# Optimization experiments

Hardware: AMD Instinct MI355X
Metric: run time of the kernel (lower is better)

## Reference

```python
import jax, jax.numpy as jnp
import numpy as np

LN_EPS = 1e-5


def _layernorm(x, w, b):
    mu = jnp.mean(x, axis=-1, keepdims=True)
    var = jnp.mean(jnp.square(x - mu), axis=-1, keepdims=True)
    return (x - mu) * jax.lax.rsqrt(var + LN_EPS) * w + b


def setup_inputs() -> dict:
    key = jax.random.key(0)
    ks = jax.random.split(key, 6)
    B, V, P, D = 32, 4, 784, 768
    H = 8
    x = jax.random.normal(ks[0], (B, V * P, D), dtype=jnp.float32)
    s = 0.02  # init scale for weights
    return {
        "x": x,
        "num_views": V,
        "norm1_w": jnp.ones((D,), jnp.float32),
        "norm1_b": jnp.zeros((D,), jnp.float32),
        "in_proj_w": jax.random.normal(ks[1], (3 * D, D), jnp.float32) * s,
        "in_proj_b": jnp.zeros((3 * D,), jnp.float32),
        "out_w": jax.random.normal(ks[2], (D, D), jnp.float32) * s,
        "out_b": jnp.zeros((D,), jnp.float32),
        "norm2_w": jnp.ones((D,), jnp.float32),
        "norm2_b": jnp.zeros((D,), jnp.float32),
        "ffn_w1": jax.random.normal(ks[3], (4 * D, D), jnp.float32) * s,
        "ffn_b1": jnp.zeros((4 * D,), jnp.float32),
        "ffn_w2": jax.random.normal(ks[4], (D, 4 * D), jnp.float32) * s,
        "ffn_b2": jnp.zeros((D,), jnp.float32),
    }


def reference(x, num_views, norm1_w, norm1_b, in_proj_w, in_proj_b, out_w, out_b,
              norm2_w, norm2_b, ffn_w1, ffn_b1, ffn_w2, ffn_b2):
    B, T, D = x.shape
    V = num_views
    P = T // V
    H = 8
    dh = D // H

    # The per-patch python loop in the original is embarrassingly parallel over
    # patches: fold the patch dim into batch -> (B*P, V, D) tokens of seq-len V.
    xv = x.reshape(B, V, P, D).transpose(0, 2, 1, 3).reshape(B * P, V, D)

    # pre-norm cross-view attention (torch MultiheadAttention, batch_first)
    h = _layernorm(xv, norm1_w, norm1_b)
    qkv = h @ in_proj_w.T + in_proj_b                      # (BP, V, 3D)
    q, k, v = jnp.split(qkv, 3, axis=-1)
    q = q.reshape(B * P, V, H, dh).transpose(0, 2, 1, 3)   # (BP, H, V, dh)
    k = k.reshape(B * P, V, H, dh).transpose(0, 2, 1, 3)
    v = v.reshape(B * P, V, H, dh).transpose(0, 2, 1, 3)
    scores = jnp.einsum("bhqd,bhkd->bhqk", q, k) / jnp.sqrt(jnp.float32(dh))
    attn = jax.nn.softmax(scores, axis=-1)
    o = jnp.einsum("bhqk,bhkd->bhqd", attn, v)             # (BP, H, V, dh)
    o = o.transpose(0, 2, 1, 3).reshape(B * P, V, D)
    o = o @ out_w.T + out_b
    xv = xv + o

    # pre-norm FFN with exact (erf) GELU; dropout = identity (eval mode)
    h = _layernorm(xv, norm2_w, norm2_b)
    h = jax.nn.gelu(h @ ffn_w1.T + ffn_b1, approximate=False)
    xv = xv + (h @ ffn_w2.T + ffn_b2)

    # undo the fold: (BP, V, D) -> (B, P, V, D) -> (B, V, P, D) -> (B, T, D)
    return xv.reshape(B, P, V, D).transpose(0, 2, 1, 3).reshape(B, T, D)
```

## Files before the change

kernel.cpp:

```cpp
#include <hip/hip_runtime.h>
#include <hip/hip_bf16.h>
#include <math.h>

typedef __bf16 bf16x8 __attribute__((ext_vector_type(8)));
typedef float  f32x4  __attribute__((ext_vector_type(4)));
typedef unsigned short us8 __attribute__((ext_vector_type(8)));
typedef unsigned short us4 __attribute__((ext_vector_type(4)));

__device__ __forceinline__ unsigned short f2bf(float x) {
  unsigned int u = __float_as_uint(x);
  u += 0x7FFFu + ((u >> 16) & 1u);
  return (unsigned short)(u >> 16);
}
__device__ __forceinline__ float bf2f(unsigned short v) {
  return __uint_as_float(((unsigned int)v) << 16);
}
__device__ __forceinline__ float gelu_t(float x) {
  float y = 0.7978845608028654f * x * (1.0f + 0.044715f * x * x);
  float e = __expf(2.0f * y);
  return x - x / (e + 1.0f);
}


__global__ __launch_bounds__(256) void conv_f32_bf16(const float* __restrict__ s,
                                                     unsigned short* __restrict__ d, int n4) {
  int i = blockIdx.x * 256 + threadIdx.x;
  if (i >= n4) return;
  float4 f = ((const float4*)s)[i];
  ushort4 u;
  u.x = f2bf(f.x); u.y = f2bf(f.y); u.z = f2bf(f.z); u.w = f2bf(f.w);
  ((ushort4*)d)[i] = u;
}

__global__ __launch_bounds__(256) void ln_kernel(const float* __restrict__ src,
                                                 const float* __restrict__ w,
                                                 const float* __restrict__ b,
                                                 unsigned short* __restrict__ dst) {
  const int wv = threadIdx.x >> 6;
  const int lane = threadIdx.x & 63;
  const int n = blockIdx.x * 4 + wv;
  const int bp = n >> 2, v = n & 3;
  const int bb = bp / 784, p = bp - bb * 784;
  const float* row = src + ((size_t)bb * 3136 + (size_t)v * 784 + p) * 768;
  float4 x0 = ((const float4*)row)[lane];
  float4 x1 = ((const float4*)row)[lane + 64];
  float4 x2 = ((const float4*)row)[lane + 128];
  float s  = x0.x + x0.y + x0.z + x0.w + x1.x + x1.y + x1.z + x1.w
           + x2.x + x2.y + x2.z + x2.w;
  float ss = x0.x*x0.x + x0.y*x0.y + x0.z*x0.z + x0.w*x0.w
           + x1.x*x1.x + x1.y*x1.y + x1.z*x1.z + x1.w*x1.w
           + x2.x*x2.x + x2.y*x2.y + x2.z*x2.z + x2.w*x2.w;
  #pragma unroll
  for (int off = 32; off > 0; off >>= 1) {
    s  += __shfl_xor(s,  off, 64);
    ss += __shfl_xor(ss, off, 64);
  }
  const float mu   = s * (1.0f / 768.0f);
  const float rstd = rsqrtf(ss * (1.0f / 768.0f) - mu * mu + 1e-5f);
  unsigned short* drow = dst + (size_t)n * 768;
  #pragma unroll
  for (int seg = 0; seg < 3; ++seg) {
    float4 xs = (seg == 0) ? x0 : (seg == 1) ? x1 : x2;
    float4 w4 = ((const float4*)w)[lane + seg * 64];
    float4 b4 = ((const float4*)b)[lane + seg * 64];
    ushort4 u;
    u.x = f2bf((xs.x - mu) * rstd * w4.x + b4.x);
    u.y = f2bf((xs.y - mu) * rstd * w4.y + b4.y);
    u.z = f2bf((xs.z - mu) * rstd * w4.z + b4.z);
    u.w = f2bf((xs.w - mu) * rstd * w4.w + b4.w);
    ((ushort4*)drow)[lane + seg * 64] = u;
  }
}

template <int K, int EPI>
__global__ __launch_bounds__(256) void gemm_k(const unsigned short* __restrict__ A,
                                              const unsigned short* __restrict__ Bm,
                                              const float* __restrict__ bias,
                                              void* __restrict__ outp,
                                              const float* __restrict__ aux,
                                              int N) {
  __shared__ unsigned short smem[2 * 128 * 64];
  unsigned short* sA = smem;
  unsigned short* sB = smem + 128 * 64;
  const int tid  = threadIdx.x;
  const int w    = tid >> 6;
  const int lane = tid & 63;
  const int quad = lane >> 4;
  const int l16  = lane & 15;
  const int wm = w >> 1, wn = w & 1;

  const int gx   = gridDim.x;
  const int flat = blockIdx.y * gx + blockIdx.x;
  const int xcd  = flat & 7;
  const int idx  = flat >> 3;
  const int iby  = idx / gx;
  const int by   = xcd * 98 + iby;
  const int bx   = idx - iby * gx;

  const int r8 = lane >> 3;
  const int cb = lane & 7;
  const int swo = ((cb ^ r8) << 3);
  const unsigned short* gA = A  + (size_t)(by * 128 + r8) * K + swo;
  const unsigned short* gB = Bm + (size_t)(bx * 128 + r8) * K + swo;

  f32x4 acc[4][4];
  #pragma unroll
  for (int i = 0; i < 4; ++i)
    #pragma unroll
    for (int j = 0; j < 4; ++j) {
      f32x4 z = {0.0f, 0.0f, 0.0f, 0.0f};
      acc[i][j] = z;
    }

  for (int k0 = 0; k0 < K; k0 += 64) {
    #pragma unroll
    for (int i = 0; i < 4; ++i) {
      const int chunk = w * 4 + i;
      __builtin_amdgcn_global_load_lds(
          (__attribute__((address_space(1))) void*)(gA + (size_t)(chunk * 8) * K + k0),
          (__attribute__((address_space(3))) void*)(&sA[chunk * 512]), 16, 0, 0);
      __builtin_amdgcn_global_load_lds(
          (__attribute__((address_space(1))) void*)(gB + (size_t)(chunk * 8) * K + k0),
          (__attribute__((address_space(3))) void*)(&sB[chunk * 512]), 16, 0, 0);
    }
    __syncthreads();

    #pragma unroll
    for (int kk = 0; kk < 2; ++kk) {
      bf16x8 af[4], bfr[4];
      const int q = kk * 4 + quad;
      #pragma unroll
      for (int mi = 0; mi < 4; ++mi) {
        const int m = wm * 64 + mi * 16 + l16;
        af[mi] = *(const bf16x8*)(&sA[m * 64 + ((q ^ (m & 7)) << 3)]);
      }
      #pragma unroll
      for (int ni = 0; ni < 4; ++ni) {
        const int n = wn * 64 + ni * 16 + l16;
        bfr[ni] = *(const bf16x8*)(&sB[n * 64 + ((q ^ (n & 7)) << 3)]);
      }
      #pragma unroll
      for (int mi = 0; mi < 4; ++mi)
        #pragma unroll
        for (int ni = 0; ni < 4; ++ni)
          acc[mi][ni] = __builtin_amdgcn_mfma_f32_16x16x32_bf16(af[mi], bfr[ni],
                                                                acc[mi][ni], 0, 0, 0);
    }
    __syncthreads();
  }

  float* lsm = (float*)smem;
  float biasv[4];
  #pragma unroll
  for (int ni = 0; ni < 4; ++ni) biasv[ni] = bias[bx * 128 + wn * 64 + ni * 16 + l16];

  #pragma unroll
  for (int hf = 0; hf < 2; ++hf) {
    if (wm == hf) {
      #pragma unroll
      for (int mi = 0; mi < 4; ++mi)
        #pragma unroll
        for (int ni = 0; ni < 4; ++ni) {
          const int col_l = wn * 64 + ni * 16 + l16;
          #pragma unroll
          for (int r = 0; r < 4; ++r) {
            const int row_l = mi * 16 + quad * 4 + r;
            lsm[row_l * 128 + col_l] = acc[mi][ni][r] + biasv[ni];
          }
        }
    }
    __syncthreads();
    #pragma unroll
    for (int j = 0; j < 8; ++j) {
      const int cc    = tid + 256 * j;
      const int row_l = cc >> 5;
      const int col4  = (cc & 31) << 2;
      f32x4 vv = *(const f32x4*)&lsm[row_l * 128 + col4];
      const int rr    = by * 128 + hf * 64 + row_l;
      const int col_g = bx * 128 + col4;
      if (EPI == 0) {
        const int seg = col_g / 768;
        const int c2  = col_g - seg * 768;
        const int hh  = c2 / 96;
        const int dd  = c2 - hh * 96;
        const int bp = rr >> 2, v = rr & 3;
        us4 u = { f2bf(vv[0]), f2bf(vv[1]), f2bf(vv[2]), f2bf(vv[3]) };
        *(us4*)((unsigned short*)outp + (size_t)bp * 9216 + seg * 3072 + hh * 384 + v * 96 + dd) = u;
      } else if (EPI == 1 || EPI == 3) {
        const int bp = rr >> 2, v = rr & 3;
        const int bb = bp / 784, p = bp - bb * 784;
        const size_t addr = ((size_t)bb * 3136 + (size_t)v * 784 + p) * 768 + col_g;
        f32x4 a4 = *(const f32x4*)(aux + addr);
        vv += a4;
        *(f32x4*)((float*)outp + addr) = vv;
      } else {
        us4 u = { f2bf(gelu_t(vv[0])), f2bf(gelu_t(vv[1])),
                  f2bf(gelu_t(vv[2])), f2bf(gelu_t(vv[3])) };
        *(us4*)((unsigned short*)outp + (size_t)rr * N + col_g) = u;
      }
    }
    __syncthreads();
  }
}

__global__ __launch_bounds__(256) void attn_kernel(const unsigned short* __restrict__ qs,
                                                   unsigned short* __restrict__ o) {
  int idx = blockIdx.x * 256 + threadIdx.x;
  int vq = idx & 3;
  int h  = (idx >> 2) & 7;
  int bp = idx >> 5;
  const unsigned short* qp = qs + (size_t)bp * 9216 + h * 384 + vq * 96;
  const unsigned short* kp = qs + (size_t)bp * 9216 + 3072 + h * 384;
  const unsigned short* vp = qs + (size_t)bp * 9216 + 6144 + h * 384;
  float s0 = 0.f, s1 = 0.f, s2 = 0.f, s3 = 0.f;
  #pragma unroll
  for (int c = 0; c < 96; c += 8) {
    us8 q8 = *(const us8*)(qp + c);
    us8 k0 = *(const us8*)(kp + c);
    us8 k1 = *(const us8*)(kp + 96 + c);
    us8 k2 = *(const us8*)(kp + 192 + c);
    us8 k3 = *(const us8*)(kp + 288 + c);
    #pragma unroll
    for (int j = 0; j < 8; ++j) {
      float qf = bf2f(q8[j]);
      s0 += qf * bf2f(k0[j]);
      s1 += qf * bf2f(k1[j]);
      s2 += qf * bf2f(k2[j]);
      s3 += qf * bf2f(k3[j]);
    }
  }
  const float scale = 0.10206207261596575f;
  s0 *= scale; s1 *= scale; s2 *= scale; s3 *= scale;
  float m = fmaxf(fmaxf(s0, s1), fmaxf(s2, s3));
  float e0 = __expf(s0 - m), e1 = __expf(s1 - m), e2 = __expf(s2 - m), e3 = __expf(s3 - m);
  float inv = 1.0f / (e0 + e1 + e2 + e3);
  e0 *= inv; e1 *= inv; e2 *= inv; e3 *= inv;
  unsigned short* op = o + (size_t)(bp * 4 + vq) * 768 + h * 96;
  #pragma unroll
  for (int c = 0; c < 96; c += 8) {
    us8 v0 = *(const us8*)(vp + c);
    us8 v1 = *(const us8*)(vp + 96 + c);
    us8 v2 = *(const us8*)(vp + 192 + c);
    us8 v3 = *(const us8*)(vp + 288 + c);
    us8 r;
    #pragma unroll
    for (int j = 0; j < 8; ++j) {
      float val = e0 * bf2f(v0[j]) + e1 * bf2f(v1[j]) + e2 * bf2f(v2[j]) + e3 * bf2f(v3[j]);
      r[j] = f2bf(val);
    }
    *(us8*)(op + c) = r;
  }
}

extern "C" void kernel_launch(void* const* d_in, const int* in_sizes, int n_in,
                              void* d_out, int out_size, void* d_ws, size_t ws_size,
                              hipStream_t stream) {
  const float* x         = (const float*)d_in[0];
  const float* norm1_w   = (const float*)d_in[2];
  const float* norm1_b   = (const float*)d_in[3];
  const float* in_proj_w = (const float*)d_in[4];
  const float* in_proj_b = (const float*)d_in[5];
  const float* out_w     = (const float*)d_in[6];
  const float* out_b     = (const float*)d_in[7];
  const float* norm2_w   = (const float*)d_in[8];
  const float* norm2_b   = (const float*)d_in[9];
  const float* ffn_w1    = (const float*)d_in[10];
  const float* ffn_b1    = (const float*)d_in[11];
  const float* ffn_w2    = (const float*)d_in[12];
  const float* ffn_b2    = (const float*)d_in[13];
  float* out = (float*)d_out;

  char* ws = (char*)d_ws;
  unsigned short* wq = (unsigned short*)ws;
  unsigned short* wh = (unsigned short*)(ws + 616562688u);
  unsigned short* wB = (unsigned short*)(ws + 616562688u + 154140672u);
  unsigned short* wIn  = wB;
  unsigned short* wOut = wB + 1769472;
  unsigned short* wF1  = wOut + 589824;
  unsigned short* wF2  = wF1 + 2359296;

  conv_f32_bf16<<<(442368 + 255) / 256, 256, 0, stream>>>(in_proj_w, wIn, 442368);
  conv_f32_bf16<<<(147456 + 255) / 256, 256, 0, stream>>>(out_w, wOut, 147456);
  conv_f32_bf16<<<(589824 + 255) / 256, 256, 0, stream>>>(ffn_w1, wF1, 589824);
  conv_f32_bf16<<<(589824 + 255) / 256, 256, 0, stream>>>(ffn_w2, wF2, 589824);

  ln_kernel<<<25088, 256, 0, stream>>>(x, norm1_w, norm1_b, wh);
  gemm_k<768, 0><<<dim3(18, 784), 256, 0, stream>>>(wh, wIn, in_proj_b, (void*)wq, nullptr, 2304);
  attn_kernel<<<3136, 256, 0, stream>>>(wq, wh);
  gemm_k<768, 1><<<dim3(6, 784), 256, 0, stream>>>(wh, wOut, out_b, (void*)out, x, 768);
  ln_kernel<<<25088, 256, 0, stream>>>(out, norm2_w, norm2_b, wh);
  gemm_k<768, 2><<<dim3(24, 784), 256, 0, stream>>>(wh, wF1, ffn_b1, (void*)wq, nullptr, 3072);
  gemm_k<3072, 3><<<dim3(6, 784), 256, 0, stream>>>(wq, wF2, ffn_b2, (void*)out, out, 768);

  (void)in_sizes; (void)n_in; (void)out_size; (void)ws_size;
}
```

Before: 3.302 ms.

## Replace 128x128 GEMM with 256x256 tile, 8-wave, double-buffered pipelined GEMM

Replaces the 128x128-tile, 4-wave GEMM with a 256x256-tile, 512-thread kernel. It double-buffers LDS (128KB) and interleaves global->LDS staging of half-tiles with MFMA compute, using explicit vmcnt waits, barriers and setprio. Bias addition moves to the vectorized epilogue. The aim is more data reuse per tile and hiding global load latency, at the cost of large LDS use (limits occupancy) and intricate synchronization that is easy to get wrong.

After: 2.644 ms. -20.0%, faster.

```diff
diff --git a/kernel.cpp b/kernel.cpp
--- a/kernel.cpp
+++ b/kernel.cpp
@@ -6,6 +6,7 @@
 typedef float  f32x4  __attribute__((ext_vector_type(4)));
 typedef unsigned short us8 __attribute__((ext_vector_type(8)));
 typedef unsigned short us4 __attribute__((ext_vector_type(4)));
+typedef unsigned short ush;
 
 __device__ __forceinline__ unsigned short f2bf(float x) {
   unsigned int u = __float_as_uint(x);
@@ -72,112 +73,166 @@
   }
 }
 
+
+#define BARX() do { asm volatile("" ::: "memory"); \
+                    __builtin_amdgcn_s_barrier();  \
+                    asm volatile("" ::: "memory"); } while (0)
+#define WAITVM(N) asm volatile("s_waitcnt vmcnt(" #N ")" ::: "memory")
+
+#define STAGE(ISB, HALF, TT) do {                                             \
+  const ush* _g = (ISB) ? gB : gA;                                            \
+  const int _l0 = (((TT) & 1) << 15) + ((ISB) ? 16384 : 0) + ((HALF) << 13)   \
+                + (w << 9);                                                   \
+  const size_t _go = (size_t)(((HALF) << 7) + (w << 3)) * K                   \
+                   + ((size_t)(TT) << 6);                                     \
+  __builtin_amdgcn_global_load_lds(                                           \
+      (const __attribute__((address_space(1))) void*)(_g + _go),              \
+      (__attribute__((address_space(3))) void*)(smem + _l0), 16, 0, 0);       \
+  __builtin_amdgcn_global_load_lds(                                           \
+      (const __attribute__((address_space(1))) void*)(_g + _go + ((size_t)K << 6)), \
+      (__attribute__((address_space(3))) void*)(smem + _l0 + 4096), 16, 0, 0);\
+} while (0)
+
+#define LDA(HM) do {                                                          \
+  _Pragma("unroll")                                                           \
+  for (int mi4 = 0; mi4 < 4; ++mi4) {                                         \
+    const int m = wm * 64 + (HM) * 128 + mi4 * 16 + l16;                      \
+    _Pragma("unroll")                                                         \
+    for (int kk = 0; kk < 2; ++kk) {                                          \
+      const int q = kk * 4 + quad;                                            \
+      af[mi4][kk] = *(const bf16x8*)(smem + aofs + m * 64 + ((q ^ l7) << 3)); \
+    }                                                                         \
+  }                                                                           \
+} while (0)
+
+#define LDB(HN, BF) do {                                                      \
+  _Pragma("unroll")                                                           \
+  for (int ni2 = 0; ni2 < 2; ++ni2) {                                         \
+    const int n = wn * 32 + (HN) * 128 + ni2 * 16 + l16;                      \
+    _Pragma("unroll")                                                         \
+    for (int kk = 0; kk < 2; ++kk) {                                          \
+      const int q = kk * 4 + quad;                                            \
+      BF[ni2][kk] = *(const bf16x8*)(smem + bofs + n * 64 + ((q ^ l7) << 3)); \
+    }                                                                         \
+  }                                                                           \
+} while (0)
+
+#define MFMAC(HM, HN, BF) do {                                                \
+  __builtin_amdgcn_s_setprio(1);                                              \
+  _Pragma("unroll")                                                           \
+  for (int mi4 = 0; mi4 < 4; ++mi4)                                           \
+    _Pragma("unroll")                                                         \
+    for (int ni2 = 0; ni2 < 2; ++ni2)                                         \
+      _Pragma("unroll")                                                       \
+      for (int kk = 0; kk < 2; ++kk)                                          \
+        acc[(HM)*4 + mi4][(HN)*2 + ni2] = __builtin_amdgcn_mfma_f32_16x16x32_bf16( \
+            af[mi4][kk], BF[ni2][kk], acc[(HM)*4 + mi4][(HN)*2 + ni2], 0, 0, 0); \
+  __builtin_amdgcn_s_setprio(0);                                              \
+} while (0)
+
 template <int K, int EPI>
-__global__ __launch_bounds__(256) void gemm_k(const unsigned short* __restrict__ A,
-                                              const unsigned short* __restrict__ Bm,
-                                              const float* __restrict__ bias,
-                                              void* __restrict__ outp,
-                                              const float* __restrict__ aux,
-                                              int N) {
-  __shared__ unsigned short smem[2 * 128 * 64];
-  unsigned short* sA = smem;
-  unsigned short* sB = smem + 128 * 64;
+__global__ __launch_bounds__(512, 2) void gemm256(const ush* __restrict__ A,
+                                                  const ush* __restrict__ Bm,
+                                                  const float* __restrict__ bias,
+                                                  void* __restrict__ outp,
+                                                  const float* __restrict__ aux,
+                                                  int N) {
+  __shared__ __attribute__((aligned(16))) ush smem[65536];
+  constexpr int NT = K / 64;
   const int tid  = threadIdx.x;
   const int w    = tid >> 6;
   const int lane = tid & 63;
   const int quad = lane >> 4;
   const int l16  = lane & 15;
-  const int wm = w >> 1, wn = w & 1;
+  const int l7   = l16 & 7;
+  const int wm   = w >> 2;
+  const int wn   = w & 3;
 
   const int gx   = gridDim.x;
+  const int nwg  = gx * 392;
   const int flat = blockIdx.y * gx + blockIdx.x;
   const int xcd  = flat & 7;
-  const int idx  = flat >> 3;
-  const int iby  = idx / gx;
-  const int by   = xcd * 98 + iby;
-  const int bx   = idx - iby * gx;
-
-  const int r8 = lane >> 3;
-  const int cb = lane & 7;
-  const int swo = ((cb ^ r8) << 3);
-  const unsigned short* gA = A  + (size_t)(by * 128 + r8) * K + swo;
-  const unsigned short* gB = Bm + (size_t)(bx * 128 + r8) * K + swo;
-
-  f32x4 acc[4][4];
-  #pragma unroll
-  for (int i = 0; i < 4; ++i)
+  const int pos  = xcd * (nwg >> 3) + (flat >> 3);
+  const int by   = pos / gx;
+  const int bx   = pos - by * gx;
+
+  const int r8  = lane >> 3;
+  const int cb  = lane & 7;
+  const int swo = (cb ^ r8) << 3;
+  const ush* gA = A  + (size_t)(by * 256 + r8) * K + swo;
+  const ush* gB = Bm + (size_t)(bx * 256 + r8) * K + swo;
+
+  f32x4 acc[8][4];
+  #pragma unroll
+  for (int i = 0; i < 8; ++i)
     #pragma unroll
     for (int j = 0; j < 4; ++j) {
       f32x4 z = {0.0f, 0.0f, 0.0f, 0.0f};
       acc[i][j] = z;
     }
-
-  for (int k0 = 0; k0 < K; k0 += 64) {
-    #pragma unroll
-    for (int i = 0; i < 4; ++i) {
-      const int chunk = w * 4 + i;
-      __builtin_amdgcn_global_load_lds(
-          (__attribute__((address_space(1))) void*)(gA + (size_t)(chunk * 8) * K + k0),
-          (__attribute__((address_space(3))) void*)(&sA[chunk * 512]), 16, 0, 0);
-      __builtin_amdgcn_global_load_lds(
-          (__attribute__((address_space(1))) void*)(gB + (size_t)(chunk * 8) * K + k0),
-          (__attribute__((address_space(3))) void*)(&sB[chunk * 512]), 16, 0, 0);
-    }
-    __syncthreads();
-
-    #pragma unroll
-    for (int kk = 0; kk < 2; ++kk) {
-      bf16x8 af[4], bfr[4];
-      const int q = kk * 4 + quad;
+  bf16x8 af[4][2], bf0[2][2], bf1[2][2];
+
+  STAGE(0, 0, 0); STAGE(1, 0, 0); STAGE(0, 1, 0);
+  STAGE(1, 1, 0); STAGE(0, 0, 1); STAGE(1, 0, 1);
+  WAITVM(8);
+  BARX();
+
+  #pragma unroll 2
+  for (int t = 0; t < NT; ++t) {
+    const int aofs = (t & 1) << 15;
+    const int bofs = aofs + 16384;
+    LDA(0); LDB(0, bf0);
+    if (t <= NT - 2) STAGE(0, 1, t + 1);
+    BARX();
+    MFMAC(0, 0, bf0);
+    if (t < NT - 1) { WAITVM(6); } else { WAITVM(0); }
+    BARX();
+    LDB(1, bf1);
+    if (t <= NT - 2) STAGE(1, 1, t + 1);
+    BARX();
+    MFMAC(0, 1, bf1);
+    BARX();
+    LDA(1);
+    if (t <= NT - 3) STAGE(0, 0, t + 2);
+    BARX();
+    MFMAC(1, 0, bf0);
+    BARX();
+    if (t <= NT - 3) STAGE(1, 0, t + 2);
+    BARX();
+    MFMAC(1, 1, bf1);
+    if (t <= NT - 3)      { WAITVM(8); }
+    else if (t == NT - 2) { WAITVM(4); }
+    BARX();
+  }
+
+  float* lsm = (float*)smem;
+  #pragma unroll
+  for (int s = 0; s < 4; ++s) {
+    if (wm == (s & 1)) {
+      const int hm = s >> 1;
       #pragma unroll
-      for (int mi = 0; mi < 4; ++mi) {
-        const int m = wm * 64 + mi * 16 + l16;
-        af[mi] = *(const bf16x8*)(&sA[m * 64 + ((q ^ (m & 7)) << 3)]);
-      }
-      #pragma unroll
-      for (int ni = 0; ni < 4; ++ni) {
-        const int n = wn * 64 + ni * 16 + l16;
-        bfr[ni] = *(const bf16x8*)(&sB[n * 64 + ((q ^ (n & 7)) << 3)]);
-      }
-      #pragma unroll
-      for (int mi = 0; mi < 4; ++mi)
-        #pragma unroll
-        for (int ni = 0; ni < 4; ++ni)
-          acc[mi][ni] = __builtin_amdgcn_mfma_f32_16x16x32_bf16(af[mi], bfr[ni],
-                                                                acc[mi][ni], 0, 0, 0);
-    }
-    __syncthreads();
-  }
-
-  float* lsm = (float*)smem;
-  float biasv[4];
-  #pragma unroll
-  for (int ni = 0; ni < 4; ++ni) biasv[ni] = bias[bx * 128 + wn * 64 + ni * 16 + l16];
-
-  #pragma unroll
-  for (int hf = 0; hf < 2; ++hf) {
-    if (wm == hf) {
-      #pragma unroll
-      for (int mi = 0; mi < 4; ++mi)
+      for (int mi4 = 0; mi4 < 4; ++mi4)
         #pragma unroll
         for (int ni = 0; ni < 4; ++ni) {
-          const int col_l = wn * 64 + ni * 16 + l16;
+          const int col = wn * 32 + (ni >> 1) * 128 + (ni & 1) * 16 + l16;
           #pragma unroll
           for (int r = 0; r < 4; ++r) {
-            const int row_l = mi * 16 + quad * 4 + r;
-            lsm[row_l * 128 + col_l] = acc[mi][ni][r] + biasv[ni];
+            const int row_l = mi4 * 16 + quad * 4 + r;
+            lsm[row_l * 260 + col] = acc[hm * 4 + mi4][ni][r];
           }
         }
     }
     __syncthreads();
     #pragma unroll
     for (int j = 0; j < 8; ++j) {
-      const int cc    = tid + 256 * j;
-      const int row_l = cc >> 5;
-      const int col4  = (cc & 31) << 2;
-      f32x4 vv = *(const f32x4*)&lsm[row_l * 128 + col4];
-      const int rr    = by * 128 + hf * 64 + row_l;
-      const int col_g = bx * 128 + col4;
+      const int cc    = tid + 512 * j;
+      const int row_l = cc >> 6;
+      const int c4    = (cc & 63) << 2;
+      f32x4 vv = *(const f32x4*)&lsm[row_l * 260 + c4];
+      const int rr    = by * 256 + s * 64 + row_l;
+      const int col_g = bx * 256 + c4;
+      f32x4 b4 = *(const f32x4*)&bias[col_g];
+      vv += b4;
       if (EPI == 0) {
         const int seg = col_g / 768;
         const int c2  = col_g - seg * 768;
@@ -285,12 +340,12 @@
   conv_f32_bf16<<<(589824 + 255) / 256, 256, 0, stream>>>(ffn_w2, wF2, 589824);
 
   ln_kernel<<<25088, 256, 0, stream>>>(x, norm1_w, norm1_b, wh);
-  gemm_k<768, 0><<<dim3(18, 784), 256, 0, stream>>>(wh, wIn, in_proj_b, (void*)wq, nullptr, 2304);
+  gemm256<768, 0><<<dim3(9, 392), 512, 0, stream>>>(wh, wIn, in_proj_b, (void*)wq, nullptr, 2304);
   attn_kernel<<<3136, 256, 0, stream>>>(wq, wh);
-  gemm_k<768, 1><<<dim3(6, 784), 256, 0, stream>>>(wh, wOut, out_b, (void*)out, x, 768);
+  gemm256<768, 1><<<dim3(3, 392), 512, 0, stream>>>(wh, wOut, out_b, (void*)out, x, 768);
   ln_kernel<<<25088, 256, 0, stream>>>(out, norm2_w, norm2_b, wh);
-  gemm_k<768, 2><<<dim3(24, 784), 256, 0, stream>>>(wh, wF1, ffn_b1, (void*)wq, nullptr, 3072);
-  gemm_k<3072, 3><<<dim3(6, 784), 256, 0, stream>>>(wq, wF2, ffn_b2, (void*)out, out, 768);
+  gemm256<768, 2><<<dim3(12, 392), 512, 0, stream>>>(wh, wF1, ffn_b1, (void*)wq, nullptr, 3072);
+  gemm256<3072, 3><<<dim3(3, 392), 512, 0, stream>>>(wq, wF2, ffn_b2, (void*)out, out, 768);
 
   (void)in_sizes; (void)n_in; (void)out_size; (void)ws_size;
 }
```
